# Optimization experiments

Measured on AMD Instinct MI355X. Metric: run time of the kernel, lower is better.

## Reference

```python
import jax, jax.numpy as jnp
import numpy as np

# --- static Cayley table for Cl(3) (8 blades) ---
def _derive_cayley_table():
    basis_gens = [(), (1,), (2,), (3,), (1, 2), (1, 3), (2, 3), (1, 2, 3)]
    gens_to_idx = {g: i for i, g in enumerate(basis_gens)}
    def reduce(a, b):
        gens = list(a) + list(b)
        sign = 1
        changed = True
        while changed:
            changed = False
            i = 0
            while i < len(gens) - 1:
                if gens[i] == gens[i + 1]:
                    gens.pop(i); gens.pop(i)
                    changed = True
                    if i > 0:
                        i -= 1
                elif gens[i] > gens[i + 1]:
                    gens[i], gens[i + 1] = gens[i + 1], gens[i]
                    sign *= -1
                    changed = True
                    i += 1
                else:
                    i += 1
        return gens_to_idx[tuple(gens)], sign
    return [[reduce(basis_gens[i], basis_gens[j]) for j in range(8)] for i in range(8)]

_TAB = _derive_cayley_table()
SI = np.array([i for i in range(8) for _ in range(8)], dtype=np.int32)
SJ = np.array([j for _ in range(8) for j in range(8)], dtype=np.int32)
TK = np.array([_TAB[i][j][0] for i in range(8) for j in range(8)], dtype=np.int32)
SG = np.array([float(_TAB[i][j][1]) for i in range(8) for j in range(8)], dtype=np.float32)

N_TOK, N_BLADE, D_BLADE, D_FFN = 8192, 8, 256, 1024
LN_EPS = 1e-5


def setup_inputs() -> dict:
    key = jax.random.key(0)
    ks = jax.random.split(key, 5)
    scale = 0.02
    return {
        'x': jax.random.normal(ks[0], (N_TOK, N_BLADE, D_BLADE), jnp.float32),
        'interaction_weights': jnp.full((64,), 0.1, jnp.float32),
        'geo_gate': jnp.asarray(0.5, jnp.float32),
        'ln_w': jnp.ones((D_BLADE,), jnp.float32),
        'ln_b': jnp.zeros((D_BLADE,), jnp.float32),
        'W_gate': jax.random.normal(ks[1], (D_BLADE, D_FFN), jnp.float32) * scale,
        'W_up': jax.random.normal(ks[2], (D_BLADE, D_FFN), jnp.float32) * scale,
        'W_down': jax.random.normal(ks[3], (D_FFN, D_BLADE), jnp.float32) * scale,
    }


def reference(x, interaction_weights, geo_gate, ln_w, ln_b, W_gate, W_up, W_down):
    si = jnp.asarray(SI); sj = jnp.asarray(SJ); tk = jnp.asarray(TK)
    sg = jnp.asarray(SG).astype(x.dtype)
    w = jax.nn.sigmoid(interaction_weights).astype(x.dtype)
    # gather blade pairs, weighted Cayley product: (N, 64, D)
    products = x[:, si, :] * x[:, sj, :] * (sg * w)[None, :, None]
    # scatter-add into target blades: (N, 8, D)
    geo = jnp.zeros_like(x).at[:, tk, :].add(products)
    g = jax.nn.sigmoid(geo_gate)
    mixed = g * geo + (1.0 - g) * x
    # LayerNorm over D
    flat = mixed.reshape(-1, x.shape[-1])
    mu = jnp.mean(flat, axis=-1, keepdims=True)
    var = jnp.var(flat, axis=-1, keepdims=True)
    flat = (flat - mu) * jax.lax.rsqrt(var + LN_EPS) * ln_w + ln_b
    # SwiGLU FFN
    h = jax.nn.silu(flat @ W_gate) * (flat @ W_up)
    out = (h @ W_down).reshape(x.shape)
    return x + out
```

## Files before the change

kernel.cpp:

```cpp
#include <hip/hip_runtime.h>
#include <hip/hip_bf16.h>
#include <hip/hip_fp8.h>

typedef __bf16 bf16x8 __attribute__((ext_vector_type(8)));
typedef float floatx4 __attribute__((ext_vector_type(4)));

constexpr int TK[64] = {
  0,1,2,3,4,5,6,7,
  1,0,4,5,2,3,7,6,
  2,4,0,6,1,7,3,5,
  3,5,6,0,7,1,2,4,
  4,2,1,7,0,6,5,3,
  5,3,7,1,6,0,4,2,
  6,7,3,2,5,4,0,1,
  7,6,5,4,3,2,1,0
};
constexpr float SGN[64] = {
  1, 1, 1, 1, 1, 1, 1, 1,
  1, 1, 1, 1, 1, 1, 1, 1,
  1,-1, 1, 1,-1,-1, 1,-1,
  1,-1,-1, 1, 1,-1,-1, 1,
  1,-1, 1, 1,-1,-1, 1,-1,
  1,-1,-1, 1, 1,-1,-1, 1,
  1, 1,-1, 1,-1, 1,-1,-1,
  1, 1,-1, 1,-1, 1,-1,-1
};

__device__ __forceinline__ void async16(const void* g, void* l) {
  __builtin_amdgcn_global_load_lds(
      (const __attribute__((address_space(1))) void*)g,
      (__attribute__((address_space(3))) void*)l, 16, 0, 0);
}

__device__ __forceinline__ unsigned char to_fp8(float v) {
  __hip_fp8_e4m3 q(v);
  return (unsigned char)q.__x;
}

__global__ __launch_bounds__(256) void transpose_cast_gu(
    const float* __restrict__ src, __bf16* __restrict__ dst, int sel)
{
  __shared__ float s[32 * 33];
  const int t = threadIdx.x;
  const int k0 = blockIdx.y * 32, f0 = blockIdx.x * 32;
  const int r = t >> 5, c = t & 31;
  #pragma unroll
  for (int i = 0; i < 4; ++i)
    s[(r + i * 8) * 33 + c] = src[(size_t)(k0 + r + i * 8) * 1024 + f0 + c];
  __syncthreads();
  #pragma unroll
  for (int i = 0; i < 4; ++i) {
    int f = f0 + r + i * 8;
    int n = ((f >> 5) << 6) + sel * 32 + (f & 31);
    dst[(size_t)n * 256 + k0 + c] = (__bf16)s[c * 33 + r + i * 8];
  }
}

__global__ __launch_bounds__(256) void transpose_cast_fp8(
    const float* __restrict__ src, unsigned char* __restrict__ dst, int K, int N)
{
  __shared__ float s[32 * 33];
  const int t = threadIdx.x;
  const int k0 = blockIdx.y * 32, n0 = blockIdx.x * 32;
  const int r = t >> 5, c = t & 31;
  #pragma unroll
  for (int i = 0; i < 4; ++i)
    s[(r + i * 8) * 33 + c] = src[(size_t)(k0 + r + i * 8) * N + n0 + c];
  __syncthreads();
  #pragma unroll
  for (int i = 0; i < 4; ++i)
    dst[(size_t)(n0 + r + i * 8) * K + k0 + c] = to_fp8(16.f * s[c * 33 + r + i * 8]);
}

__global__ __launch_bounds__(256) void geo_ln(
    const float* __restrict__ X,
    const float* __restrict__ IW,
    const float* __restrict__ GG,
    const float* __restrict__ LW, const float* __restrict__ LB,
    __bf16* __restrict__ F)
{
  __shared__ float sw[64];
  __shared__ float smix[8 * 256];
  __shared__ float sstat[16];
  const int t = threadIdx.x;
  const int tok = blockIdx.x;

  if (t < 64) sw[t] = SGN[t] / (1.f + __expf(-IW[t]));

  float xv[8];
  #pragma unroll
  for (int b = 0; b < 8; ++b) xv[b] = X[(size_t)tok * 2048 + b * 256 + t];
  const float g = 1.f / (1.f + __expf(-GG[0]));

  __syncthreads();

  float geo[8] = {0.f, 0.f, 0.f, 0.f, 0.f, 0.f, 0.f, 0.f};
  #pragma unroll
  for (int p = 0; p < 64; ++p)
    geo[TK[p]] += xv[p >> 3] * xv[p & 7] * sw[p];

  float mv[8];
  #pragma unroll
  for (int b = 0; b < 8; ++b) {
    mv[b] = g * geo[b] + (1.f - g) * xv[b];
    smix[b * 256 + t] = mv[b];
  }
  __syncthreads();

  const int wv = t >> 6, lane = t & 63;
  #pragma unroll
  for (int s = 0; s < 2; ++s) {
    int b = wv * 2 + s;
    float v0 = smix[b * 256 + lane];
    float v1 = smix[b * 256 + 64 + lane];
    float v2 = smix[b * 256 + 128 + lane];
    float v3 = smix[b * 256 + 192 + lane];
    float sum = v0 + v1 + v2 + v3;
    float sq  = v0*v0 + v1*v1 + v2*v2 + v3*v3;
    #pragma unroll
    for (int off = 32; off > 0; off >>= 1) {
      sum += __shfl_xor(sum, off, 64);
      sq  += __shfl_xor(sq,  off, 64);
    }
    if (lane == 0) {
      float mu  = sum * (1.f / 256.f);
      float var = sq * (1.f / 256.f) - mu * mu;
      sstat[b]     = mu;
      sstat[8 + b] = rsqrtf(var + 1e-5f);
    }
  }
  __syncthreads();

  const float lw = LW[t], lb = LB[t];
  #pragma unroll
  for (int b = 0; b < 8; ++b) {
    float v = (mv[b] - sstat[b]) * sstat[8 + b] * lw + lb;
    F[(size_t)(tok * 8 + b) * 256 + t] = (__bf16)v;
  }
}

__global__ __launch_bounds__(512, 2) void gemm_gateup(
    const __bf16* __restrict__ A,
    const __bf16* __restrict__ B,
    unsigned char* __restrict__ H)
{
  __shared__ __align__(16) char smc[65536];

  const int t = threadIdx.x;
  const int l = t & 63;
  const int wv = t >> 6, wm = wv & 1, wn = wv >> 1;
  const int j4 = l >> 4;

  const int bid = blockIdx.x;
  const int lid = (bid & 7) * 256 + (bid >> 3);
  const int m0 = (lid >> 3) * 256;
  const int n0 = (lid & 7) * 256;

  const int rA = t >> 3;
  const int rB = ((t >> 8) * 64) + ((t & 255) >> 3);
  const int cs = ((t & 7) ^ ((t >> 3) & 7)) * 8;
  const __bf16* gA = A + (size_t)(m0 + rA) * 256 + cs;
  const __bf16* gB = B + (size_t)(n0 + rB) * 256 + cs;
  char* dA = smc + t * 16;
  char* dB = smc + 32768 + (t >> 8) * 4096 + t * 16;

#define STAGE_AE(KT) { async16(gA + (KT), dA);                 async16(gA + 32768 + (KT), dA + 16384); }
#define STAGE_AO(KT) { async16(gA + 16384 + (KT), dA + 8192);  async16(gA + 49152 + (KT), dA + 24576); }
#define STAGE_BE(KT) { async16(gB + (KT), dB);                 async16(gB + 32768 + (KT), dB + 16384); }
#define STAGE_BO(KT) { async16(gB + 8192 + (KT), dB + 4096);   async16(gB + 40960 + (KT), dB + 20480); }

  const int rbA = (wm * 128 + (l & 15)) * 128;
  const int rbB = 32768 + (wn * 64 + (l & 15)) * 128;
  const int sw0 = (j4 ^ (l & 7)) * 16;
  const int sw1 = ((4 + j4) ^ (l & 7)) * 16;
  const char* pA0 = smc + rbA + sw0;
  const char* pA1 = smc + rbA + sw1;
  const char* pB0 = smc + rbB + sw0;
  const char* pB1 = smc + rbB + sw1;

  bf16x8 aE[4][2], aO[4][2], bE[2][2], bO[2][2];
  floatx4 acc[8][4];
  #pragma unroll
  for (int i = 0; i < 8; ++i)
    #pragma unroll
    for (int j = 0; j < 4; ++j)
      acc[i][j] = floatx4{0.f, 0.f, 0.f, 0.f};

#define MFMA_QUAD(av, bv, mo, no)                                         \
  _Pragma("unroll")                                                       \
  for (int kk = 0; kk < 2; ++kk)                                          \
    _Pragma("unroll")                                                     \
    for (int mi = 0; mi < 4; ++mi)                                        \
      _Pragma("unroll")                                                   \
      for (int nj = 0; nj < 2; ++nj)                                      \
        acc[(mo) + mi][(no) + nj] = __builtin_amdgcn_mfma_f32_16x16x32_bf16( \
            av[mi][kk], bv[nj][kk], acc[(mo) + mi][(no) + nj], 0, 0, 0);

#define PHASE_MID()                                          \
  __builtin_amdgcn_s_barrier();                              \
  asm volatile("s_waitcnt lgkmcnt(0)" ::: "memory");         \
  __builtin_amdgcn_sched_barrier(0);                         \
  __builtin_amdgcn_s_setprio(1);

#define PHASE_TAIL()                                         \
  __builtin_amdgcn_s_setprio(0);                             \
  __builtin_amdgcn_sched_barrier(0);

  STAGE_AE(0); STAGE_BE(0); STAGE_BO(0); STAGE_AO(0);
  asm volatile("s_waitcnt vmcnt(4)" ::: "memory");
  __builtin_amdgcn_s_barrier();

  #pragma unroll
  for (int kt = 0; kt < 4; ++kt) {
    const int ktn = (kt + 1) * 64;

    #pragma unroll
    for (int mi = 0; mi < 4; ++mi) {
      aE[mi][0] = *(const bf16x8*)(pA0 + mi * 2048);
      aE[mi][1] = *(const bf16x8*)(pA1 + mi * 2048);
    }
    #pragma unroll
    for (int nj = 0; nj < 2; ++nj) {
      bE[nj][0] = *(const bf16x8*)(pB0 + nj * 2048);
      bE[nj][1] = *(const bf16x8*)(pB1 + nj * 2048);
    }
    PHASE_MID();
    MFMA_QUAD(aE, bE, 0, 0);
    PHASE_TAIL();
    asm volatile("s_waitcnt vmcnt(2)" ::: "memory");
    __builtin_amdgcn_s_barrier();

    #pragma unroll
    for (int nj = 0; nj < 2; ++nj) {
      bO[nj][0] = *(const bf16x8*)(pB0 + 4096 + nj * 2048);
      bO[nj][1] = *(const bf16x8*)(pB1 + 4096 + nj * 2048);
    }
    if (kt < 3) { STAGE_AE(ktn); STAGE_BE(ktn); }
    PHASE_MID();
    MFMA_QUAD(aE, bO, 0, 2);
    PHASE_TAIL();
    if (kt < 3) { asm volatile("s_waitcnt vmcnt(4)" ::: "memory"); }
    else        { asm volatile("s_waitcnt vmcnt(0)" ::: "memory"); }
    __builtin_amdgcn_s_barrier();

    #pragma unroll
    for (int mi = 0; mi < 4; ++mi) {
      aO[mi][0] = *(const bf16x8*)(pA0 + 8192 + mi * 2048);
      aO[mi][1] = *(const bf16x8*)(pA1 + 8192 + mi * 2048);
    }
    if (kt < 3) STAGE_BO(ktn);
    PHASE_MID();
    MFMA_QUAD(aO, bE, 4, 0);
    PHASE_TAIL();
    __builtin_amdgcn_s_barrier();

    if (kt < 3) STAGE_AO(ktn);
    PHASE_MID();
    MFMA_QUAD(aO, bO, 4, 2);
    PHASE_TAIL();
    if (kt < 3) {
      asm volatile("s_waitcnt vmcnt(4)" ::: "memory");
      __builtin_amdgcn_s_barrier();
    }
  }

  __syncthreads();
  unsigned char* sH = (unsigned char*)smc;
  #pragma unroll
  for (int mi = 0; mi < 8; ++mi)
    #pragma unroll
    for (int nj = 0; nj < 2; ++nj) {
      floatx4 gv4 = acc[mi][nj], uv4 = acc[mi][nj + 2];
      int fcol = wn * 32 + nj * 16 + (l & 15);
      #pragma unroll
      for (int r = 0; r < 4; ++r) {
        int mloc = wm * 128 + mi * 16 + j4 * 4 + r;
        float gvv = gv4[r], uvv = uv4[r];
        float hv = (gvv / (1.f + __expf(-gvv))) * uvv;
        sH[mloc * 128 + fcol] = to_fp8(16.f * hv);
      }
    }
  __syncthreads();
  const size_t hbase = (size_t)m0 * 1024 + (n0 >> 1);
  #pragma unroll
  for (int c = 0; c < 4; ++c) {
    int chunk = c * 512 + t;
    int mloc = chunk >> 3, col = chunk & 7;
    *(int4*)&H[hbase + (size_t)mloc * 1024 + col * 16] =
        *(const int4*)&sH[mloc * 128 + col * 16];
  }
#undef STAGE_AE
#undef STAGE_AO
#undef STAGE_BE
#undef STAGE_BO
#undef MFMA_QUAD
#undef PHASE_MID
#undef PHASE_TAIL
}

__global__ __launch_bounds__(256, 2) void gemm_down(
    const unsigned char* __restrict__ A,
    const unsigned char* __restrict__ B,
    const float* __restrict__ X,
    float* __restrict__ O)
{
  __shared__ unsigned char sA[128 * 64];
  __shared__ unsigned char sB[256 * 64];
  const int t = threadIdx.x;
  const int m0 = blockIdx.x * 128;
  const int lane = t & 63, wv = t >> 6;
  const int wm = wv & 1, wn = wv >> 1;
  const int l15 = lane & 15, quad = lane >> 4;

  int aoff[2], boff[4];
  #pragma unroll
  for (int i = 0; i < 2; ++i) {
    int idx = i * 256 + t, row = idx >> 2, q = idx & 3;
    aoff[i] = (m0 + row) * 1024 + (q ^ ((row >> 1) & 3)) * 16;
  }
  #pragma unroll
  for (int i = 0; i < 4; ++i) {
    int idx = i * 256 + t, row = idx >> 2, q = idx & 3;
    boff[i] = row * 1024 + (q ^ ((row >> 1) & 3)) * 16;
  }

  floatx4 zero = {0.f, 0.f, 0.f, 0.f};
  floatx4 acc[4][8];
  #pragma unroll
  for (int i = 0; i < 4; ++i)
    #pragma unroll
    for (int j = 0; j < 8; ++j) acc[i][j] = zero;

  int aaddr[2][4], baddr[2][8];
  #pragma unroll
  for (int s = 0; s < 2; ++s) {
    const int u = s * 4 + quad;
    #pragma unroll
    for (int i = 0; i < 4; ++i) {
      int r = wm * 64 + i * 16 + l15;
      aaddr[s][i] = r * 64 + (((u >> 1) ^ ((r >> 1) & 3)) << 4) + (u & 1) * 8;
    }
    #pragma unroll
    for (int j = 0; j < 8; ++j) {
      int r = wn * 128 + j * 16 + l15;
      baddr[s][j] = r * 64 + (((u >> 1) ^ ((r >> 1) & 3)) << 4) + (u & 1) * 8;
    }
  }

  for (int k = 0; k < 16; ++k) {
    const int kk = k * 64;
    #pragma unroll
    for (int i = 0; i < 2; ++i) async16(A + aoff[i] + kk, &sA[(i * 256 + t) * 16]);
    #pragma unroll
    for (int i = 0; i < 4; ++i) async16(B + boff[i] + kk, &sB[(i * 256 + t) * 16]);
    __syncthreads();

    #pragma unroll
    for (int s = 0; s < 2; ++s) {
      long av[4], bv[8];
      #pragma unroll
      for (int i = 0; i < 4; ++i) av[i] = *(const long*)&sA[aaddr[s][i]];
      #pragma unroll
      for (int j = 0; j < 8; ++j) bv[j] = *(const long*)&sB[baddr[s][j]];
      #pragma unroll
      for (int i = 0; i < 4; ++i)
        #pragma unroll
        for (int j = 0; j < 8; ++j)
          acc[i][j] = __builtin_amdgcn_mfma_f32_16x16x32_fp8_fp8(av[i], bv[j], acc[i][j], 0, 0, 0);
    }
    __syncthreads();
  }

  #pragma unroll
  for (int i = 0; i < 4; ++i)
    #pragma unroll
    for (int j = 0; j < 8; ++j)
      #pragma unroll
      for (int r = 0; r < 4; ++r) {
        int m = m0 + wm * 64 + i * 16 + quad * 4 + r;
        int n = wn * 128 + j * 16 + l15;
        size_t o = (size_t)m * 256 + n;
        O[o] = X[o] + acc[i][j][r] * (1.f / 256.f);
      }
}

extern "C" void kernel_launch(void* const* d_in, const int* in_sizes, int n_in,
                              void* d_out, int out_size, void* d_ws, size_t ws_size,
                              hipStream_t stream) {
  const float* x   = (const float*)d_in[0];
  const float* iw  = (const float*)d_in[1];
  const float* gg  = (const float*)d_in[2];
  const float* lnw = (const float*)d_in[3];
  const float* lnb = (const float*)d_in[4];
  const float* Wg  = (const float*)d_in[5];
  const float* Wu  = (const float*)d_in[6];
  const float* Wd  = (const float*)d_in[7];
  float* out = (float*)d_out;

  char* ws = (char*)d_ws;
  __bf16*        flat = (__bf16*)(ws);
  unsigned char* h    = (unsigned char*)(ws + 33554432);
  __bf16*        Bil  = (__bf16*)(ws + 100663296);
  unsigned char* Bd   = (unsigned char*)(ws + 101711872);

  transpose_cast_gu<<<dim3(32, 8), 256, 0, stream>>>(Wg, Bil, 0);
  transpose_cast_gu<<<dim3(32, 8), 256, 0, stream>>>(Wu, Bil, 1);
  transpose_cast_fp8<<<dim3(8, 32), 256, 0, stream>>>(Wd, Bd, 1024, 256);
  geo_ln<<<8192, 256, 0, stream>>>(x, iw, gg, lnw, lnb, flat);
  gemm_gateup<<<2048, 512, 0, stream>>>(flat, Bil, h);
  gemm_down<<<512, 256, 0, stream>>>(h, Bd, x, out);
}
```

Before: 281.7 us.

## Double-buffer gate/up GEMM LDS tiles and reorder quadrant schedule

The gate/up GEMM now uses 128KB of LDS split into two ping-pong buffers. Tiles for step T+2 are prefetched while step T computes, replacing the single-buffer half-tile staging. Each wave's M/N quadrants are remapped to interleaved halves, the MFMA quadrant order is changed to reuse loaded A/B fragments, and the weight packing interleave changes from 32 to 16 columns to match. The larger LDS footprint likely drops occupancy to one block per CU despite launch_bounds(512,2).

```diff
diff --git a/kernel.cpp b/kernel.cpp
--- a/kernel.cpp
+++ b/kernel.cpp
@@ -51,7 +51,7 @@
   #pragma unroll
   for (int i = 0; i < 4; ++i) {
     int f = f0 + r + i * 8;
-    int n = ((f >> 5) << 6) + sel * 32 + (f & 31);
+    int n = ((f >> 4) << 5) + sel * 16 + (f & 15);
     dst[(size_t)n * 256 + k0 + c] = (__bf16)s[c * 33 + r + i * 8];
   }
 }
@@ -144,41 +144,35 @@
     const __bf16* __restrict__ B,
     unsigned char* __restrict__ H)
 {
-  __shared__ __align__(16) char smc[65536];
+  __shared__ __align__(16) char smc[131072];
 
   const int t = threadIdx.x;
   const int l = t & 63;
   const int wv = t >> 6, wm = wv & 1, wn = wv >> 1;
-  const int j4 = l >> 4;
+  const int l15 = l & 15, j4 = l >> 4;
 
   const int bid = blockIdx.x;
   const int lid = (bid & 7) * 256 + (bid >> 3);
   const int m0 = (lid >> 3) * 256;
   const int n0 = (lid & 7) * 256;
 
-  const int rA = t >> 3;
-  const int rB = ((t >> 8) * 64) + ((t & 255) >> 3);
   const int cs = ((t & 7) ^ ((t >> 3) & 7)) * 8;
-  const __bf16* gA = A + (size_t)(m0 + rA) * 256 + cs;
-  const __bf16* gB = B + (size_t)(n0 + rB) * 256 + cs;
-  char* dA = smc + t * 16;
-  char* dB = smc + 32768 + (t >> 8) * 4096 + t * 16;
-
-#define STAGE_AE(KT) { async16(gA + (KT), dA);                 async16(gA + 32768 + (KT), dA + 16384); }
-#define STAGE_AO(KT) { async16(gA + 16384 + (KT), dA + 8192);  async16(gA + 49152 + (KT), dA + 24576); }
-#define STAGE_BE(KT) { async16(gB + (KT), dB);                 async16(gB + 32768 + (KT), dB + 16384); }
-#define STAGE_BO(KT) { async16(gB + 8192 + (KT), dB + 4096);   async16(gB + 40960 + (KT), dB + 20480); }
-
-  const int rbA = (wm * 128 + (l & 15)) * 128;
-  const int rbB = 32768 + (wn * 64 + (l & 15)) * 128;
-  const int sw0 = (j4 ^ (l & 7)) * 16;
-  const int sw1 = ((4 + j4) ^ (l & 7)) * 16;
-  const char* pA0 = smc + rbA + sw0;
-  const char* pA1 = smc + rbA + sw1;
-  const char* pB0 = smc + rbB + sw0;
-  const char* pB1 = smc + rbB + sw1;
-
-  bf16x8 aE[4][2], aO[4][2], bE[2][2], bO[2][2];
+  const __bf16* gA = A + (size_t)(m0 + (t >> 3)) * 256 + cs;
+  const __bf16* gB = B + (size_t)(n0 + (t >> 3)) * 256 + cs;
+
+#define STAGE_A(p, h, kt) {                                                        \
+  async16(gA + (h) * 32768 + (kt) * 64,         smc + (p) * 65536 + (h) * 16384 + t * 16);        \
+  async16(gA + (h) * 32768 + 16384 + (kt) * 64, smc + (p) * 65536 + (h) * 16384 + 8192 + t * 16); }
+#define STAGE_B(p, h, kt) {                                                        \
+  async16(gB + (h) * 32768 + (kt) * 64,         smc + (p) * 65536 + 32768 + (h) * 16384 + t * 16);        \
+  async16(gB + (h) * 32768 + 16384 + (kt) * 64, smc + (p) * 65536 + 32768 + (h) * 16384 + 8192 + t * 16); }
+
+  const int sw0 = (j4 ^ (l15 & 7)) * 16;
+  const int sw1 = ((4 + j4) ^ (l15 & 7)) * 16;
+  const char* pAr = smc + (wm * 64 + l15) * 128;
+  const char* pBr = smc + 32768 + (wn * 32 + l15) * 128;
+
+  bf16x8 aF[4][2], bE[2][2], bO[2][2];
   floatx4 acc[8][4];
   #pragma unroll
   for (int i = 0; i < 8; ++i)
@@ -186,7 +180,20 @@
     for (int j = 0; j < 4; ++j)
       acc[i][j] = floatx4{0.f, 0.f, 0.f, 0.f};
 
-#define MFMA_QUAD(av, bv, mo, no)                                         \
+#define READ_A(mh, p)                                                              \
+  _Pragma("unroll")                                                                \
+  for (int mi = 0; mi < 4; ++mi) {                                                 \
+    aF[mi][0] = *(const bf16x8*)(pAr + (p) * 65536 + (mh) * 16384 + mi * 2048 + sw0); \
+    aF[mi][1] = *(const bf16x8*)(pAr + (p) * 65536 + (mh) * 16384 + mi * 2048 + sw1); \
+  }
+#define READ_B(dst, nh, p)                                                         \
+  _Pragma("unroll")                                                                \
+  for (int nj = 0; nj < 2; ++nj) {                                                 \
+    dst[nj][0] = *(const bf16x8*)(pBr + (p) * 65536 + (nh) * 16384 + nj * 2048 + sw0); \
+    dst[nj][1] = *(const bf16x8*)(pBr + (p) * 65536 + (nh) * 16384 + nj * 2048 + sw1); \
+  }
+
+#define MFMA16(av, bv, mo, no)                                            \
   _Pragma("unroll")                                                       \
   for (int kk = 0; kk < 2; ++kk)                                          \
     _Pragma("unroll")                                                     \
@@ -196,90 +203,66 @@
         acc[(mo) + mi][(no) + nj] = __builtin_amdgcn_mfma_f32_16x16x32_bf16( \
             av[mi][kk], bv[nj][kk], acc[(mo) + mi][(no) + nj], 0, 0, 0);
 
-#define PHASE_MID()                                          \
+#define DO_MFMA(av, bv, mo, no)                              \
   __builtin_amdgcn_s_barrier();                              \
   asm volatile("s_waitcnt lgkmcnt(0)" ::: "memory");         \
   __builtin_amdgcn_sched_barrier(0);                         \
-  __builtin_amdgcn_s_setprio(1);
-
-#define PHASE_TAIL()                                         \
+  __builtin_amdgcn_s_setprio(1);                             \
+  MFMA16(av, bv, mo, no);                                    \
   __builtin_amdgcn_s_setprio(0);                             \
   __builtin_amdgcn_sched_barrier(0);
 
-  STAGE_AE(0); STAGE_BE(0); STAGE_BO(0); STAGE_AO(0);
-  asm volatile("s_waitcnt vmcnt(4)" ::: "memory");
+  STAGE_A(0, 0, 0); STAGE_B(0, 0, 0); STAGE_B(0, 1, 0); STAGE_A(0, 1, 0);
+  STAGE_A(1, 0, 1); STAGE_B(1, 0, 1); STAGE_B(1, 1, 1);
+  asm volatile("s_waitcnt vmcnt(6)" ::: "memory");
   __builtin_amdgcn_s_barrier();
 
   #pragma unroll
-  for (int kt = 0; kt < 4; ++kt) {
-    const int ktn = (kt + 1) * 64;
-
-    #pragma unroll
-    for (int mi = 0; mi < 4; ++mi) {
-      aE[mi][0] = *(const bf16x8*)(pA0 + mi * 2048);
-      aE[mi][1] = *(const bf16x8*)(pA1 + mi * 2048);
-    }
-    #pragma unroll
-    for (int nj = 0; nj < 2; ++nj) {
-      bE[nj][0] = *(const bf16x8*)(pB0 + nj * 2048);
-      bE[nj][1] = *(const bf16x8*)(pB1 + nj * 2048);
-    }
-    PHASE_MID();
-    MFMA_QUAD(aE, bE, 0, 0);
-    PHASE_TAIL();
-    asm volatile("s_waitcnt vmcnt(2)" ::: "memory");
+  for (int T = 0; T < 4; ++T) {
+    const int p = T & 1, q = p ^ 1;
+
+    READ_A(0, p);
+    READ_B(bE, 0, p);
+    if (T + 1 < 4) STAGE_A(q, 1, T + 1);
+    asm volatile("s_waitcnt lgkmcnt(8)" ::: "memory");
+    DO_MFMA(aF, bE, 0, 0);
     __builtin_amdgcn_s_barrier();
 
-    #pragma unroll
-    for (int nj = 0; nj < 2; ++nj) {
-      bO[nj][0] = *(const bf16x8*)(pB0 + 4096 + nj * 2048);
-      bO[nj][1] = *(const bf16x8*)(pB1 + 4096 + nj * 2048);
-    }
-    if (kt < 3) { STAGE_AE(ktn); STAGE_BE(ktn); }
-    PHASE_MID();
-    MFMA_QUAD(aE, bO, 0, 2);
-    PHASE_TAIL();
-    if (kt < 3) { asm volatile("s_waitcnt vmcnt(4)" ::: "memory"); }
-    else        { asm volatile("s_waitcnt vmcnt(0)" ::: "memory"); }
+    READ_B(bO, 1, p);
+    if (T + 2 < 4) STAGE_A(p, 0, T + 2);
+    DO_MFMA(aF, bO, 0, 2);
     __builtin_amdgcn_s_barrier();
 
-    #pragma unroll
-    for (int mi = 0; mi < 4; ++mi) {
-      aO[mi][0] = *(const bf16x8*)(pA0 + 8192 + mi * 2048);
-      aO[mi][1] = *(const bf16x8*)(pA1 + 8192 + mi * 2048);
-    }
-    if (kt < 3) STAGE_BO(ktn);
-    PHASE_MID();
-    MFMA_QUAD(aO, bE, 4, 0);
-    PHASE_TAIL();
+    READ_A(1, p);
+    if (T + 2 < 4) STAGE_B(p, 0, T + 2);
+    DO_MFMA(aF, bO, 4, 2);
     __builtin_amdgcn_s_barrier();
 
-    if (kt < 3) STAGE_AO(ktn);
-    PHASE_MID();
-    MFMA_QUAD(aO, bO, 4, 2);
-    PHASE_TAIL();
-    if (kt < 3) {
-      asm volatile("s_waitcnt vmcnt(4)" ::: "memory");
-      __builtin_amdgcn_s_barrier();
-    }
+    if (T + 2 < 4) STAGE_B(p, 1, T + 2);
+    DO_MFMA(aF, bE, 4, 0);
+    if (T < 2)       { asm volatile("s_waitcnt vmcnt(6)" ::: "memory"); }
+    else if (T == 2) { asm volatile("s_waitcnt vmcnt(0)" ::: "memory"); }
+    __builtin_amdgcn_s_barrier();
   }
 
   __syncthreads();
   unsigned char* sH = (unsigned char*)smc;
   #pragma unroll
-  for (int mi = 0; mi < 8; ++mi)
-    #pragma unroll
-    for (int nj = 0; nj < 2; ++nj) {
-      floatx4 gv4 = acc[mi][nj], uv4 = acc[mi][nj + 2];
-      int fcol = wn * 32 + nj * 16 + (l & 15);
+  for (int mi8 = 0; mi8 < 8; ++mi8) {
+    const int mh = mi8 >> 2, mi = mi8 & 3;
+    #pragma unroll
+    for (int nh = 0; nh < 2; ++nh) {
+      floatx4 gv4 = acc[mi8][nh * 2], uv4 = acc[mi8][nh * 2 + 1];
+      int fcol = (nh * 4 + wn) * 16 + l15;
       #pragma unroll
       for (int r = 0; r < 4; ++r) {
-        int mloc = wm * 128 + mi * 16 + j4 * 4 + r;
+        int mloc = mh * 128 + wm * 64 + mi * 16 + j4 * 4 + r;
         float gvv = gv4[r], uvv = uv4[r];
         float hv = (gvv / (1.f + __expf(-gvv))) * uvv;
         sH[mloc * 128 + fcol] = to_fp8(16.f * hv);
       }
     }
+  }
   __syncthreads();
   const size_t hbase = (size_t)m0 * 1024 + (n0 >> 1);
   #pragma unroll
@@ -289,13 +272,12 @@
     *(int4*)&H[hbase + (size_t)mloc * 1024 + col * 16] =
         *(const int4*)&sH[mloc * 128 + col * 16];
   }
-#undef STAGE_AE
-#undef STAGE_AO
-#undef STAGE_BE
-#undef STAGE_BO
-#undef MFMA_QUAD
-#undef PHASE_MID
-#undef PHASE_TAIL
+#undef STAGE_A
+#undef STAGE_B
+#undef READ_A
+#undef READ_B
+#undef MFMA16
+#undef DO_MFMA
 }
 
 __global__ __launch_bounds__(256, 2) void gemm_down(
```

Result: no change. 281.5 us (-0.1%).
